# Kernel optimization log

Hardware: AMD Instinct MI355X
Metric: run time of the kernel (lower is better)

## Reference

```python
import jax, jax.numpy as jnp
import numpy as np

N = 20000      # nodes
E = 640000     # edges
R = 90         # relations
IN_F = 128     # raw feature dim
HID = 64       # hidden_channels
OUT = 32       # out_channels of conv2
NCLASS = 4
NB = 35        # num_bases (conv1)
EPS = 1e-16    # PyG softmax epsilon


def setup_inputs() -> dict:
    key = jax.random.key(0)
    ks = jax.random.split(key, 16)
    s = 0.1
    return {
        "x": jax.random.normal(ks[0], (N, IN_F), jnp.float32),
        "edge_index": jax.random.randint(ks[1], (2, E), 0, N, jnp.int32),
        "edge_type": jax.random.randint(ks[2], (E,), 0, R, jnp.int32),
        "edge_attr": jax.random.normal(ks[3], (E, 16), jnp.float32),
        # lin1: in_channels -> hidden (no bias)
        "lin1_w": jax.random.normal(ks[4], (IN_F, HID), jnp.float32) * s,
        # conv1: basis decomposition, heads=2, out=20, dim=2 -> H*O=40, H*dim=4
        "att1": jax.random.normal(ks[5], (R, NB), jnp.float32) * s,
        "basis1": jax.random.normal(ks[6], (NB, HID, 40), jnp.float32) * s,
        "q1": jax.random.normal(ks[7], (40, 4), jnp.float32) * s,
        "k1": jax.random.normal(ks[8], (40, 4), jnp.float32) * s,
        "wmod1": jnp.ones((20,), jnp.float32),            # mod='additive' weight (init ones)
        "bias1": jnp.zeros((80,), jnp.float32),            # concat bias: H*dim*O = 80
        # conv2: block-diagonal, in=80, blocks=2, H*O=64, H*dim=2
        "w2": jax.random.normal(ks[9], (R, 2, 40, 32), jnp.float32) * s,
        "q2": jax.random.normal(ks[10], (64, 2), jnp.float32) * s,
        "k2": jax.random.normal(ks[11], (64, 2), jnp.float32) * s,
        "lin_edge_w": jax.random.normal(ks[12], (16, 64), jnp.float32) * s,
        "e2": jax.random.normal(ks[13], (64, 2), jnp.float32) * s,
        # lin2: 2*out -> nclass
        "lin2_w": jax.random.normal(ks[14], (2 * OUT, NCLASS), jnp.float32) * s,
        "lin2_b": jnp.zeros((NCLASS,), jnp.float32),
    }


def segment_softmax(alpha, seg, num_segments):
    # PyG softmax: exp(x - detach(segment_max)) / (segment_sum + 1e-16)
    m = jax.ops.segment_max(alpha, seg, num_segments=num_segments)
    e = jnp.exp(alpha - jax.lax.stop_gradient(m)[seg])
    ssum = jax.ops.segment_sum(e, seg, num_segments=num_segments)
    return e / (ssum[seg] + EPS)


def rgat_forward(x, edge_index, edge_type, edge_attr, lin1_w, att1, basis1,
                 q1, k1, wmod1, bias1, w2, q2, k2, lin_edge_w, e2, lin2_w, lin2_b):
    src, dst = edge_index[0], edge_index[1]   # x_j = x[src], x_i = x[dst]
    n = x.shape[0]
    e = src.shape[0]

    h = x @ lin1_w                            # [N, HID]

    # ---- conv1: basis decomposition, within-relation, multiplicative attn, mod='additive'
    w = jnp.einsum('rb,bio->rio', att1, basis1)          # [R, HID, 40]
    xw = jnp.einsum('ni,rio->rno', h, w)                 # [R, N, 40] (all-relation transform)
    outj = xw[edge_type, src]                            # [E, 40]
    outi = xw[edge_type, dst]                            # [E, 40]
    qi = outi @ q1                                       # [E, 4]
    kj = outj @ k1                                       # [E, 4]
    alpha = qi * kj                                      # multiplicative-self-attention
    seg = dst.astype(jnp.int32) * R + edge_type          # within-relation softmax groups
    alpha = segment_softmax(alpha, seg, n * R)           # [E, 4]
    outj4 = outj.reshape(e, 2, 1, 20)                    # [E, H, 1, O]
    hmod = wmod1 * jnp.broadcast_to(outj4, (e, 2, 2, 20))  # mod='additive' term
    msg = outj4 * alpha.reshape(e, 2, 2, 1) + hmod       # [E, H, dim, O]
    agg = jax.ops.segment_sum(msg, dst, num_segments=n)  # [N, 2, 2, 20]
    h1 = agg.reshape(n, 80) + bias1
    h1 = jax.nn.relu(h1)

    # ---- conv2: block-diagonal, across-relation, additive attn, edge features, no bias
    xb = h1.reshape(n, 2, 40)
    xw2 = jnp.einsum('nbc,rbcd->rnbd', xb, w2).reshape(R, n, 64)  # [R, N, 64]
    outj = xw2[edge_type, src]                           # [E, 64]
    outi = xw2[edge_type, dst]
    qi = outi @ q2                                       # [E, 2]
    kj = outj @ k2
    ae = (edge_attr @ lin_edge_w) @ e2                   # [E, 2]
    alpha = jax.nn.leaky_relu(qi + kj + ae, 0.2)         # additive-self-attention
    alpha = segment_softmax(alpha, dst, n)               # across-relation
    msg = alpha.reshape(e, 2, 1) * outj.reshape(e, 2, 32)
    h2 = jax.ops.segment_sum(msg, dst, num_segments=n).reshape(n, 64)

    out = h2 @ lin2_w + lin2_b
    return jax.nn.log_softmax(out, axis=-1)


def reference(x, edge_index, edge_type, edge_attr, lin1_w, att1, basis1, q1, k1,
              wmod1, bias1, w2, q2, k2, lin_edge_w, e2, lin2_w, lin2_b):
    return rgat_forward(x, edge_index, edge_type, edge_attr, lin1_w, att1, basis1,
                        q1, k1, wmod1, bias1, w2, q2, k2, lin_edge_w, e2, lin2_w, lin2_b)
```

## Files before the change

kernel.cpp:

```cpp
#include <hip/hip_runtime.h>
#include <math.h>

constexpr int NN   = 20000;
constexpr int EE   = 640000;
constexpr int RR   = 90;
constexpr int INF_ = 128;
constexpr int HID  = 64;
constexpr float EPS = 1e-16f;
constexpr int E2   = 646144;

typedef unsigned short u16;
typedef _Float16 f16;
typedef __attribute__((ext_vector_type(8))) short bf16x8;
typedef __attribute__((ext_vector_type(8))) _Float16 f16x8;
typedef __attribute__((ext_vector_type(4))) _Float16 f16x4;
typedef __attribute__((ext_vector_type(4))) float f32x4;

__device__ inline u16 f2bf(float f) {
    unsigned int u = __float_as_uint(f);
    unsigned int r = (u + 0x7FFFu + ((u >> 16) & 1u)) >> 16;
    return (u16)r;
}

__device__ inline unsigned f2ord(float f) {
    unsigned u = __float_as_uint(f);
    return (u & 0x80000000u) ? ~u : (u | 0x80000000u);
}
__device__ inline float ord2f(unsigned x) {
    unsigned u = (x & 0x80000000u) ? (x & 0x7FFFFFFFu) : ~x;
    return __uint_as_float(u);
}
#define ORD_NEGINF 0x007FFFFFu

__global__ void k_fillrec(int4* p, int n) {
    int i = blockIdx.x * blockDim.x + threadIdx.x;
    if (i < n) { int4 r; r.x = 0; r.y = 0; r.z = 0; r.w = -1; p[i] = r; }
}

__global__ void k_hist(const int* et, int* hist) {
    __shared__ int lh[RR];
    if (threadIdx.x < RR) lh[threadIdx.x] = 0;
    __syncthreads();
    int i = blockIdx.x * blockDim.x + threadIdx.x;
    if (i < EE) atomicAdd(&lh[et[i]], 1);
    __syncthreads();
    if (threadIdx.x < RR) atomicAdd(&hist[threadIdx.x], lh[threadIdx.x]);
}

__global__ void k_scanPad(const int* hist, int* cursor) {
    if (threadIdx.x == 0) {
        int acc = 0;
        for (int r = 0; r < RR; ++r) {
            cursor[r] = acc;
            acc += (hist[r] + 63) & ~63;
        }
    }
}

__global__ void k_scatter(const int* src, const int* dst, const int* et,
                          int* cursor, int4* sortedR, int* posS) {
    __shared__ int lh[RR];
    __shared__ int lbase[RR];
    if (threadIdx.x < RR) lh[threadIdx.x] = 0;
    __syncthreads();
    int i = blockIdx.x * blockDim.x + threadIdx.x;
    int r = et[i];
    int rank = atomicAdd(&lh[r], 1);
    __syncthreads();
    if (threadIdx.x < RR) {
        int c = lh[threadIdx.x];
        lbase[threadIdx.x] = c ? atomicAdd(&cursor[threadIdx.x], c) : 0;
    }
    __syncthreads();
    int pos = lbase[r] + rank;
    int4 rec; rec.x = src[i]; rec.y = dst[i]; rec.z = r; rec.w = i;
    sortedR[pos] = rec;
    posS[i] = pos;
}

__global__ void k_histD(const int* dst, int* histD) {
    int i = blockIdx.x * blockDim.x + threadIdx.x;
    if (i < EE) atomicAdd(&histD[dst[i]], 1);
}

__global__ void k_scanD(const int* histD, int* rowptrD, int* cursorD) {
    __shared__ int part[256];
    const int CH = (NN + 255) / 256;
    int tid = threadIdx.x;
    int base = tid * CH;
    int s = 0;
    for (int j = 0; j < CH; ++j) {
        int idx = base + j;
        if (idx < NN) s += histD[idx];
    }
    part[tid] = s;
    __syncthreads();
    if (tid == 0) {
        int acc = 0;
        for (int t = 0; t < 256; ++t) { int v = part[t]; part[t] = acc; acc += v; }
    }
    __syncthreads();
    int acc = part[tid];
    for (int j = 0; j < CH; ++j) {
        int idx = base + j;
        if (idx < NN) {
            rowptrD[idx] = acc;
            cursorD[idx] = acc;
            acc += histD[idx];
        }
    }
    if (tid == 0) rowptrD[NN] = EE;
}

__global__ void k_scatterD(const int4* sortedR, int* cursorD, int* posD,
                           u16* relD) {
    int i = blockIdx.x * blockDim.x + threadIdx.x;
    if (i >= E2) return;
    int4 rec = sortedR[i];
    if (rec.w < 0) return;
    int pos = atomicAdd(&cursorD[rec.y], 1);
    posD[i] = pos;
    relD[pos] = (u16)rec.z;
}

__global__ void k_w1(const float* att1, const float* basis1, float* w1) {
    int idx = blockIdx.x * blockDim.x + threadIdx.x;
    if (idx >= RR * 2560) return;
    int r = idx / 2560, co = idx - r * 2560;
    float acc = 0.f;
    for (int b = 0; b < 35; ++b) acc += att1[r * 35 + b] * basis1[b * 2560 + co];
    w1[idx] = acc;
}

__global__ void k_wqk1(const float* w1, const float* q1, const float* k1,
                       float* wq1, float* wk1) {
    int idx = blockIdx.x * blockDim.x + threadIdx.x;
    if (idx >= RR * 64 * 4) return;
    int t = idx & 3, c = (idx >> 2) & 63, r = idx >> 8;
    const float* wrow = w1 + (size_t)r * 2560 + c * 40;
    float aq = 0.f, ak = 0.f;
    for (int o = 0; o < 40; ++o) {
        float w = wrow[o];
        aq += w * q1[o * 4 + t];
        ak += w * k1[o * 4 + t];
    }
    wq1[idx] = aq; wk1[idx] = ak;
}

__global__ void k_wqk2(const float* w2, const float* q2, const float* k2,
                       float* wq2, float* wk2) {
    int idx = blockIdx.x * blockDim.x + threadIdx.x;
    if (idx >= RR * 80 * 2) return;
    int t = idx & 1, bc = (idx >> 1) % 80, r = idx / 160;
    int b = bc / 40, c = bc % 40;
    const float* wbase = w2 + (size_t)((r * 2 + b) * 40 + c) * 32;
    float aq = 0.f, ak = 0.f;
    for (int d = 0; d < 32; ++d) {
        float w = wbase[d];
        aq += w * q2[(b * 32 + d) * 2 + t];
        ak += w * k2[(b * 32 + d) * 2 + t];
    }
    wq2[idx] = aq; wk2[idx] = ak;
}

__global__ void k_we(const float* lew, const float* e2, float* we) {
    int idx = threadIdx.x;
    if (idx >= 32) return;
    int i = idx >> 1, t = idx & 1;
    float acc = 0.f;
    for (int j = 0; j < 64; ++j) acc += lew[i * 64 + j] * e2[j * 2 + t];
    we[idx] = acc;
}

__global__ __launch_bounds__(256) void k_ae(const float* ea, const float* weg,
                                            const int* posS, float* aeS) {
    __shared__ float wes[32];
    if (threadIdx.x < 32) wes[threadIdx.x] = weg[threadIdx.x];
    __syncthreads();
    int e = blockIdx.x * 256 + threadIdx.x;
    if (e >= EE) return;
    const float4* ep = (const float4*)(ea + (size_t)e * 16);
    float a0 = 0.f, a1 = 0.f;
#pragma unroll
    for (int cc = 0; cc < 4; ++cc) {
        float4 v = ep[cc];
        const float* vv = (const float*)&v;
#pragma unroll
        for (int j = 0; j < 4; ++j) {
            int ii = cc * 4 + j;
            a0 = fmaf(vv[j], wes[ii * 2 + 0], a0);
            a1 = fmaf(vv[j], wes[ii * 2 + 1], a1);
        }
    }
    float2 av; av.x = a0; av.y = a1;
    *(float2*)(aeS + (size_t)posS[e] * 2) = av;
}

__global__ void k_w1bT(const float* w1, u16* w1bT) {
    int idx = blockIdx.x * blockDim.x + threadIdx.x;
    if (idx >= RR * 48 * 64) return;
    int k = idx & 63, o = (idx >> 6) % 48, r = idx / (48 * 64);
    float v = (o < 40) ? w1[(size_t)r * 2560 + k * 40 + o] : 0.f;
    w1bT[idx] = f2bf(v);
}

__global__ void k_w2bT(const float* w2, u16* w2bT) {
    int idx = blockIdx.x * blockDim.x + threadIdx.x;
    if (idx >= RR * 2 * 32 * 64) return;
    int c = idx & 63, d = (idx >> 6) & 31, b = (idx >> 11) & 1, r = idx >> 12;
    float v = (c < 40) ? w2[((((size_t)r * 2 + b) * 40) + c) * 32 + d] : 0.f;
    w2bT[idx] = f2bf(v);
}

__global__ void k_h(const float* x, const float* lin1_w, f16* hh, u16* hb) {
    __shared__ float xs[INF_];
    int n = blockIdx.x, t = threadIdx.x;
    xs[t]      = x[(size_t)n * INF_ + t];
    xs[t + 64] = x[(size_t)n * INF_ + t + 64];
    __syncthreads();
    float acc = 0.f;
    for (int i = 0; i < INF_; ++i) acc += xs[i] * lin1_w[i * HID + t];
    hh[(size_t)n * HID + t] = (f16)acc;
    hb[(size_t)n * HID + t] = f2bf(acc);
}

__device__ __forceinline__ void attn1_compute(const f16x8* hd, const f16x8* hs,
                                              const float* __restrict__ q,
                                              const float* __restrict__ k,
                                              float* qi, float* kj) {
#pragma unroll
    for (int t = 0; t < 4; ++t) { qi[t] = 0.f; kj[t] = 0.f; }
#pragma unroll
    for (int cc = 0; cc < 8; ++cc) {
        f16x8 a = hd[cc], b = hs[cc];
#pragma unroll
        for (int j = 0; j < 8; ++j) {
            float av = (float)a[j];
            float bv = (float)b[j];
            const float* q4 = q + (cc * 8 + j) * 4;
            const float* k4 = k + (cc * 8 + j) * 4;
#pragma unroll
            for (int t = 0; t < 4; ++t) {
                qi[t] = fmaf(av, q4[t], qi[t]);
                kj[t] = fmaf(bv, k4[t], kj[t]);
            }
        }
    }
}

__global__ __launch_bounds__(256) void k_e1s(const int4* sortedR, const f16* hh,
                                             const float* wq1g, const float* wk1g,
                                             const int* posD, float* alpha1s) {
    __shared__ float qs[256], ks[256];
    int i = blockIdx.x * 256 + threadIdx.x;
    int4 ed = sortedR[i];
    int s = ed.x, d = ed.y, r = ed.z;
    int rFirst = sortedR[(size_t)blockIdx.x * 256].z;
    int rLast  = sortedR[(size_t)blockIdx.x * 256 + 255].z;
    bool allsame = (rFirst == rLast);
    if (allsame) {
        qs[threadIdx.x] = wq1g[(size_t)rFirst * 256 + threadIdx.x];
        ks[threadIdx.x] = wk1g[(size_t)rFirst * 256 + threadIdx.x];
    }
    __syncthreads();
    if (ed.w < 0) return;
    const f16x8* hd = (const f16x8*)(hh + (size_t)d * 64);
    const f16x8* hs = (const f16x8*)(hh + (size_t)s * 64);
    float qi[4], kj[4];
    if (allsame) attn1_compute(hd, hs, qs, ks, qi, kj);
    else         attn1_compute(hd, hs, wq1g + (size_t)r * 256, wk1g + (size_t)r * 256, qi, kj);
    float4 av;
    av.x = qi[0] * kj[0];
    av.y = qi[1] * kj[1];
    av.z = qi[2] * kj[2];
    av.w = qi[3] * kj[3];
    *(float4*)(alpha1s + (size_t)posD[i] * 4) = av;
}

__global__ __launch_bounds__(256) void k_mfma1(const int4* sortedR, const int* posD,
                                               const u16* hb, const u16* w1bT,
                                               f16* outj1h) {
    int wid = threadIdx.x >> 6, l = threadIdx.x & 63;
    int base = blockIdx.x * 64;
    int r = sortedR[base].z;
    int e0 = base + wid * 16;
    int row16 = l & 15, g = l >> 4;
    bf16x8 a[3][2];
#pragma unroll
    for (int mt = 0; mt < 3; ++mt)
#pragma unroll
        for (int ks = 0; ks < 2; ++ks)
            a[mt][ks] = *(const bf16x8*)(w1bT + ((size_t)r * 48 + mt * 16 + row16) * 64 + ks * 32 + g * 8);
    int4 er = sortedR[e0 + row16];
    int s = er.x;
    bf16x8 b0 = *(const bf16x8*)(hb + (size_t)s * 64 + g * 8);
    bf16x8 b1 = *(const bf16x8*)(hb + (size_t)s * 64 + 32 + g * 8);
    f32x4 acc[3];
#pragma unroll
    for (int mt = 0; mt < 3; ++mt) acc[mt] = (f32x4){0.f, 0.f, 0.f, 0.f};
#pragma unroll
    for (int mt = 0; mt < 3; ++mt) {
        acc[mt] = __builtin_amdgcn_mfma_f32_16x16x32_bf16(a[mt][0], b0, acc[mt], 0, 0, 0);
        acc[mt] = __builtin_amdgcn_mfma_f32_16x16x32_bf16(a[mt][1], b1, acc[mt], 0, 0, 0);
    }
    if (er.w < 0) return;
    int pd = posD[e0 + row16];
    f16* orow = outj1h + (size_t)pd * 40;
#pragma unroll
    for (int mt = 0; mt < 3; ++mt) {
        int col = mt * 16 + g * 4;
        if (col < 40) {
            f16x4 v;
            v[0] = (f16)acc[mt][0]; v[1] = (f16)acc[mt][1];
            v[2] = (f16)acc[mt][2]; v[3] = (f16)acc[mt][3];
            *(f16x4*)(orow + col) = v;
        }
    }
}

__global__ __launch_bounds__(256) void k_aggr1(const u16* relD, const int* rowptrD,
                                               const f16* outj1h, const float* alpha1s,
                                               const float* wmod, const float* bias1,
                                               f16* h1h, u16* h1b) {
    __shared__ unsigned smax[4][RR * 5];
    __shared__ float    ssum[4][RR * 5];
    int wid = threadIdx.x >> 6;
    int lane = threadIdx.x & 63;
    int w = blockIdx.x * 4 + wid;
    int beg = rowptrD[w], end = rowptrD[w + 1];
    unsigned* mx = smax[wid];
    float*    sm = ssum[wid];
    for (int j = beg + lane; j < end; j += 64) {
        int rb = relD[j] * 5;
        mx[rb + 0] = ORD_NEGINF; mx[rb + 1] = ORD_NEGINF;
        mx[rb + 2] = ORD_NEGINF; mx[rb + 3] = ORD_NEGINF;
        sm[rb + 0] = 0.f; sm[rb + 1] = 0.f; sm[rb + 2] = 0.f; sm[rb + 3] = 0.f;
    }
    __syncthreads();
    for (int j = beg + lane; j < end; j += 64) {
        float4 a = *(const float4*)(alpha1s + (size_t)j * 4);
        int rb = relD[j] * 5;
        atomicMax(&mx[rb + 0], f2ord(a.x));
        atomicMax(&mx[rb + 1], f2ord(a.y));
        atomicMax(&mx[rb + 2], f2ord(a.z));
        atomicMax(&mx[rb + 3], f2ord(a.w));
    }
    __syncthreads();
    for (int j = beg + lane; j < end; j += 64) {
        float4 a = *(const float4*)(alpha1s + (size_t)j * 4);
        int rb = relD[j] * 5;
        atomicAdd(&sm[rb + 0], __expf(a.x - ord2f(mx[rb + 0])));
        atomicAdd(&sm[rb + 1], __expf(a.y - ord2f(mx[rb + 1])));
        atomicAdd(&sm[rb + 2], __expf(a.z - ord2f(mx[rb + 2])));
        atomicAdd(&sm[rb + 3], __expf(a.w - ord2f(mx[rb + 3])));
    }
    __syncthreads();
    for (int t = lane; t < RR * 5; t += 64) sm[t] = 1.f / (sm[t] + EPS);
    __syncthreads();
    int hh2 = lane >= 20 ? 1 : 0;
    int oo = lane - hh2 * 20;
    float acc0 = 0.f, acc1 = 0.f, accw = 0.f;
    if (lane < 40) {
        for (int j = beg; j < end; ++j) {
            int rb = relD[j] * 5 + hh2 * 2;
            float v = (float)outj1h[(size_t)j * 40 + lane];
            float2 a = *(const float2*)(alpha1s + (size_t)j * 4 + hh2 * 2);
            float e0 = __expf(a.x - ord2f(mx[rb]));
            float e1 = __expf(a.y - ord2f(mx[rb + 1]));
            acc0 = fmaf(v, e0 * sm[rb], acc0);
            acc1 = fmaf(v, e1 * sm[rb + 1], acc1);
            accw += v;
        }
        float wm = wmod[oo];
        int b0 = hh2 * 40 + oo;
        float o0 = fmaxf(acc0 + wm * accw + bias1[b0], 0.f);
        float o1 = fmaxf(acc1 + wm * accw + bias1[b0 + 20], 0.f);
        h1h[(size_t)w * 80 + b0]      = (f16)o0;
        h1h[(size_t)w * 80 + b0 + 20] = (f16)o1;
        h1b[((size_t)w * 2 + hh2) * 64 + oo]      = f2bf(o0);
        h1b[((size_t)w * 2 + hh2) * 64 + oo + 20] = f2bf(o1);
    } else {
        int lam = lane - 40;
        h1b[((size_t)w * 2 + 0) * 64 + 40 + lam] = 0;
        h1b[((size_t)w * 2 + 1) * 64 + 40 + lam] = 0;
    }
}

__device__ __forceinline__ void attn2_compute(const f16x8* hd, const f16x8* hs,
                                              const float* __restrict__ q,
                                              const float* __restrict__ k,
                                              float* a) {
    a[0] = 0.f; a[1] = 0.f;
#pragma unroll
    for (int cc = 0; cc < 10; ++cc) {
        f16x8 xv = hd[cc], yv = hs[cc];
#pragma unroll
        for (int j = 0; j < 8; ++j) {
            float x = (float)xv[j];
            float y = (float)yv[j];
            int bc = cc * 8 + j;
            a[0] = fmaf(x, q[bc * 2 + 0], fmaf(y, k[bc * 2 + 0], a[0]));
            a[1] = fmaf(x, q[bc * 2 + 1], fmaf(y, k[bc * 2 + 1], a[1]));
        }
    }
}

__global__ __launch_bounds__(256) void k_f1s(const int4* sortedR, const f16* h1h,
                                             const float* wq2g, const float* wk2g,
                                             const float* aeS, const int* posD,
                                             float* alpha2s) {
    __shared__ float qs[160], ks[160];
    int i = blockIdx.x * 256 + threadIdx.x;
    int4 ed = sortedR[i];
    int s = ed.x, d = ed.y, r = ed.z, e = ed.w;
    int rFirst = sortedR[(size_t)blockIdx.x * 256].z;
    int rLast  = sortedR[(size_t)blockIdx.x * 256 + 255].z;
    bool allsame = (rFirst == rLast);
    if (allsame && threadIdx.x < 160) {
        qs[threadIdx.x] = wq2g[(size_t)rFirst * 160 + threadIdx.x];
        ks[threadIdx.x] = wk2g[(size_t)rFirst * 160 + threadIdx.x];
    }
    __syncthreads();
    if (e < 0) return;
    const f16x8* hd = (const f16x8*)(h1h + (size_t)d * 80);
    const f16x8* hs = (const f16x8*)(h1h + (size_t)s * 80);
    float a[2];
    if (allsame) attn2_compute(hd, hs, qs, ks, a);
    else         attn2_compute(hd, hs, wq2g + (size_t)r * 160, wk2g + (size_t)r * 160, a);
    float2 aev = *(const float2*)(aeS + (size_t)i * 2);
    a[0] += aev.x;
    a[1] += aev.y;
    a[0] = a[0] > 0.f ? a[0] : 0.2f * a[0];
    a[1] = a[1] > 0.f ? a[1] : 0.2f * a[1];
    float2 av; av.x = a[0]; av.y = a[1];
    *(float2*)(alpha2s + (size_t)posD[i] * 2) = av;
}

__global__ __launch_bounds__(256) void k_mfma2(const int4* sortedR, const int* posD,
                                               const u16* h1b, const u16* w2bT,
                                               f16* outj2h) {
    int wid = threadIdx.x >> 6, l = threadIdx.x & 63;
    int base = blockIdx.x * 64;
    int r = sortedR[base].z;
    int e0 = base + wid * 16;
    int row16 = l & 15, g = l >> 4;
    bf16x8 a[2][2][2];
#pragma unroll
    for (int b = 0; b < 2; ++b)
#pragma unroll
        for (int mt = 0; mt < 2; ++mt)
#pragma unroll
            for (int ks = 0; ks < 2; ++ks)
                a[b][mt][ks] = *(const bf16x8*)(w2bT + ((((size_t)r * 2 + b) * 32) + mt * 16 + row16) * 64 + ks * 32 + g * 8);
    int4 er = sortedR[e0 + row16];
    int s = er.x;
    bf16x8 bb[2][2];
#pragma unroll
    for (int b = 0; b < 2; ++b)
#pragma unroll
        for (int ks = 0; ks < 2; ++ks)
            bb[b][ks] = *(const bf16x8*)(h1b + ((size_t)s * 2 + b) * 64 + ks * 32 + g * 8);
    f32x4 acc[2][2];
#pragma unroll
    for (int b = 0; b < 2; ++b)
#pragma unroll
        for (int mt = 0; mt < 2; ++mt) acc[b][mt] = (f32x4){0.f, 0.f, 0.f, 0.f};
#pragma unroll
    for (int b = 0; b < 2; ++b)
#pragma unroll
        for (int mt = 0; mt < 2; ++mt) {
            acc[b][mt] = __builtin_amdgcn_mfma_f32_16x16x32_bf16(a[b][mt][0], bb[b][0], acc[b][mt], 0, 0, 0);
            acc[b][mt] = __builtin_amdgcn_mfma_f32_16x16x32_bf16(a[b][mt][1], bb[b][1], acc[b][mt], 0, 0, 0);
        }
    if (er.w < 0) return;
    int pd = posD[e0 + row16];
    f16* orow = outj2h + (size_t)pd * 64;
#pragma unroll
    for (int b = 0; b < 2; ++b)
#pragma unroll
        for (int mt = 0; mt < 2; ++mt) {
            f16x4 v;
            v[0] = (f16)acc[b][mt][0]; v[1] = (f16)acc[b][mt][1];
            v[2] = (f16)acc[b][mt][2]; v[3] = (f16)acc[b][mt][3];
            *(f16x4*)(orow + b * 32 + mt * 16 + g * 4) = v;
        }
}

__global__ __launch_bounds__(256) void k_aggr2(const int* rowptrD, const f16* outj2h,
                                               const float* alpha2s, float* h2) {
    int w = blockIdx.x * 4 + (threadIdx.x >> 6);
    int lane = threadIdx.x & 63;
    if (w >= NN) return;
    int beg = rowptrD[w], end = rowptrD[w + 1];
    float m0 = -INFINITY, m1 = -INFINITY;
    for (int j = beg + lane; j < end; j += 64) {
        float2 a = *(const float2*)(alpha2s + (size_t)j * 2);
        m0 = fmaxf(m0, a.x); m1 = fmaxf(m1, a.y);
    }
#pragma unroll
    for (int off = 32; off; off >>= 1) {
        m0 = fmaxf(m0, __shfl_xor(m0, off));
        m1 = fmaxf(m1, __shfl_xor(m1, off));
    }
    float s0 = 0.f, s1 = 0.f;
    for (int j = beg + lane; j < end; j += 64) {
        float2 a = *(const float2*)(alpha2s + (size_t)j * 2);
        s0 += __expf(a.x - m0); s1 += __expf(a.y - m1);
    }
#pragma unroll
    for (int off = 32; off; off >>= 1) {
        s0 += __shfl_xor(s0, off);
        s1 += __shfl_xor(s1, off);
    }
    int b = lane >> 5;
    float mb = b ? m1 : m0;
    float rs = 1.f / ((b ? s1 : s0) + EPS);
    float acc = 0.f;
    for (int j = beg; j < end; ++j) {
        float v = (float)outj2h[(size_t)j * 64 + lane];
        float a = alpha2s[(size_t)j * 2 + b];
        acc = fmaf(v, __expf(a - mb) * rs, acc);
    }
    h2[(size_t)w * 64 + lane] = acc;
}

__global__ void k_out(const float* h2, const float* lin2_w, const float* lin2_b,
                      float* out) {
    int n = blockIdx.x * blockDim.x + threadIdx.x;
    if (n >= NN) return;
    float o[4] = {lin2_b[0], lin2_b[1], lin2_b[2], lin2_b[3]};
    const float* hr = h2 + (size_t)n * 64;
    for (int c = 0; c < 64; ++c) {
        float hv = hr[c];
#pragma unroll
        for (int t = 0; t < 4; ++t) o[t] = fmaf(hv, lin2_w[c * 4 + t], o[t]);
    }
    float m = fmaxf(fmaxf(o[0], o[1]), fmaxf(o[2], o[3]));
    float s = __expf(o[0] - m) + __expf(o[1] - m) + __expf(o[2] - m) + __expf(o[3] - m);
    float lse = m + logf(s);
#pragma unroll
    for (int t = 0; t < 4; ++t) out[(size_t)n * 4 + t] = o[t] - lse;
}

extern "C" void kernel_launch(void* const* d_in, const int* in_sizes, int n_in,
                              void* d_out, int out_size, void* d_ws, size_t ws_size,
                              hipStream_t stream) {
    const float* x        = (const float*)d_in[0];
    const int*   eidx     = (const int*)d_in[1];
    const int*   etype    = (const int*)d_in[2];
    const float* eattr    = (const float*)d_in[3];
    const float* lin1_w   = (const float*)d_in[4];
    const float* att1     = (const float*)d_in[5];
    const float* basis1   = (const float*)d_in[6];
    const float* q1       = (const float*)d_in[7];
    const float* k1       = (const float*)d_in[8];
    const float* wmod1    = (const float*)d_in[9];
    const float* bias1    = (const float*)d_in[10];
    const float* w2       = (const float*)d_in[11];
    const float* q2       = (const float*)d_in[12];
    const float* k2       = (const float*)d_in[13];
    const float* lew      = (const float*)d_in[14];
    const float* e2i      = (const float*)d_in[15];
    const float* lin2_w   = (const float*)d_in[16];
    const float* lin2_b   = (const float*)d_in[17];

    const int* src = eidx;
    const int* dst = eidx + EE;

    float* W = (float*)d_ws;
    float* w1      = W;   W += 230400;
    float* wq1     = W;   W += 23040;
    float* wk1     = W;   W += 23040;
    float* wq2     = W;   W += 14400;
    float* wk2     = W;   W += 14400;
    float* we      = W;   W += 32;
    float* h2      = W;   W += (size_t)NN * 64;
    float* aeS     = W;   W += (size_t)E2 * 2;
    f16*   hh      = (f16*)W;   W += (size_t)NN * 64 / 2;
    f16*   h1h     = (f16*)W;   W += (size_t)NN * 80 / 2;
    u16*   hb      = (u16*)W;   W += (size_t)NN * 64 / 2;
    u16*   h1b     = (u16*)W;   W += (size_t)NN * 128 / 2;
    u16*   w1bT    = (u16*)W;   W += (size_t)RR * 48 * 64 / 2;
    u16*   w2bT    = (u16*)W;   W += (size_t)RR * 2 * 32 * 64 / 2;
    float* uni     = W;   W += (size_t)EE * 20 + (size_t)EE * 4;
    f16*   outj1h  = (f16*)uni;
    float* alpha1s = uni + (size_t)EE * 20;
    f16*   outj2h  = (f16*)uni;
    W += (size_t)EE * 8;
    float* alpha2s = W;   W += (size_t)EE * 2;
    int4*  sortedR = (int4*)W;
    int*   I = (int*)W;   I += (size_t)E2 * 4;
    u16*   relD    = (u16*)I;   I += (size_t)E2 / 2;
    int*   posS    = I;   I += EE;
    int*   posD    = I;   I += E2;
    int*   rowptrD = I;   I += NN + 1;
    int*   cursorD = I;   I += NN;
    int*   histD   = I;   I += NN;
    int*   hist    = I;   I += 128;
    int*   cursor  = I;   I += 128;

    hipMemsetAsync(histD, 0, (size_t)(NN + 256) * 4, stream);
    k_fillrec<<<E2 / 256, 256, 0, stream>>>(sortedR, E2);

    k_hist<<<EE / 256, 256, 0, stream>>>(etype, hist);
    k_scanPad<<<1, 64, 0, stream>>>(hist, cursor);
    k_scatter<<<EE / 256, 256, 0, stream>>>(src, dst, etype, cursor, sortedR, posS);
    k_histD<<<EE / 256, 256, 0, stream>>>(dst, histD);
    k_scanD<<<1, 256, 0, stream>>>(histD, rowptrD, cursorD);
    k_scatterD<<<E2 / 256, 256, 0, stream>>>(sortedR, cursorD, posD, relD);

    k_w1<<<(RR * 2560 + 255) / 256, 256, 0, stream>>>(att1, basis1, w1);
    k_wqk1<<<(RR * 256 + 255) / 256, 256, 0, stream>>>(w1, q1, k1, wq1, wk1);
    k_wqk2<<<(RR * 160 + 255) / 256, 256, 0, stream>>>(w2, q2, k2, wq2, wk2);
    k_we<<<1, 32, 0, stream>>>(lew, e2i, we);
    k_ae<<<EE / 256, 256, 0, stream>>>(eattr, we, posS, aeS);
    k_w1bT<<<(RR * 48 * 64) / 256, 256, 0, stream>>>(w1, w1bT);
    k_w2bT<<<(RR * 2 * 32 * 64) / 256, 256, 0, stream>>>(w2, w2bT);
    k_h<<<NN, 64, 0, stream>>>(x, lin1_w, hh, hb);

    k_e1s<<<E2 / 256, 256, 0, stream>>>(sortedR, hh, wq1, wk1, posD, alpha1s);
    k_mfma1<<<E2 / 64, 256, 0, stream>>>(sortedR, posD, hb, w1bT, outj1h);
    k_aggr1<<<NN / 4, 256, 0, stream>>>(relD, rowptrD, outj1h, alpha1s,
                                        wmod1, bias1, h1h, h1b);

    k_f1s<<<E2 / 256, 256, 0, stream>>>(sortedR, h1h, wq2, wk2, aeS, posD, alpha2s);
    k_mfma2<<<E2 / 64, 256, 0, stream>>>(sortedR, posD, h1b, w2bT, outj2h);
    k_aggr2<<<(NN + 3) / 4, 256, 0, stream>>>(rowptrD, outj2h, alpha2s, h2);

    k_out<<<(NN + 255) / 256, 256, 0, stream>>>(h2, lin2_w, lin2_b, (float*)d_out);
}
```

Measured before the change: 640.5 us.

## Fuse attention-score and MFMA message kernels per layer using fp16 operands

Merges the per-edge attention-score kernels (k_e1s/k_f1s) into the MFMA message-transform kernels, so each edge's source and destination features are loaded once. The score reduction is spread across lanes and combined with cross-lane shuffles. MFMA operands change from bf16 to fp16, which removes the duplicate bf16 copies of h, h1 and the weights. The dst-sorted position is stored in the sorted record's w field instead of a separate posD array. This saves several kernel launches and extra global traffic, but the h1h row reads now run past the 40-wide block, so a small zeroed tail pad is added.

```diff
diff --git a/kernel.cpp b/kernel.cpp
--- a/kernel.cpp
+++ b/kernel.cpp
@@ -11,16 +11,9 @@
 
 typedef unsigned short u16;
 typedef _Float16 f16;
-typedef __attribute__((ext_vector_type(8))) short bf16x8;
 typedef __attribute__((ext_vector_type(8))) _Float16 f16x8;
 typedef __attribute__((ext_vector_type(4))) _Float16 f16x4;
 typedef __attribute__((ext_vector_type(4))) float f32x4;
-
-__device__ inline u16 f2bf(float f) {
-    unsigned int u = __float_as_uint(f);
-    unsigned int r = (u + 0x7FFFu + ((u >> 16) & 1u)) >> 16;
-    return (u16)r;
-}
 
 __device__ inline unsigned f2ord(float f) {
     unsigned u = __float_as_uint(f);
@@ -112,14 +105,13 @@
     if (tid == 0) rowptrD[NN] = EE;
 }
 
-__global__ void k_scatterD(const int4* sortedR, int* cursorD, int* posD,
-                           u16* relD) {
+__global__ void k_scatterD(int4* sortedR, int* cursorD, u16* relD) {
     int i = blockIdx.x * blockDim.x + threadIdx.x;
     if (i >= E2) return;
     int4 rec = sortedR[i];
     if (rec.w < 0) return;
     int pos = atomicAdd(&cursorD[rec.y], 1);
-    posD[i] = pos;
+    ((int*)(sortedR + i))[3] = pos;
     relD[pos] = (u16)rec.z;
 }
 
@@ -196,23 +188,23 @@
     *(float2*)(aeS + (size_t)posS[e] * 2) = av;
 }
 
-__global__ void k_w1bT(const float* w1, u16* w1bT) {
+__global__ void k_w1hT(const float* w1, f16* w1hT) {
     int idx = blockIdx.x * blockDim.x + threadIdx.x;
     if (idx >= RR * 48 * 64) return;
     int k = idx & 63, o = (idx >> 6) % 48, r = idx / (48 * 64);
     float v = (o < 40) ? w1[(size_t)r * 2560 + k * 40 + o] : 0.f;
-    w1bT[idx] = f2bf(v);
-}
-
-__global__ void k_w2bT(const float* w2, u16* w2bT) {
+    w1hT[idx] = (f16)v;
+}
+
+__global__ void k_w2hT(const float* w2, f16* w2hT) {
     int idx = blockIdx.x * blockDim.x + threadIdx.x;
     if (idx >= RR * 2 * 32 * 64) return;
     int c = idx & 63, d = (idx >> 6) & 31, b = (idx >> 11) & 1, r = idx >> 12;
     float v = (c < 40) ? w2[((((size_t)r * 2 + b) * 40) + c) * 32 + d] : 0.f;
-    w2bT[idx] = f2bf(v);
-}
-
-__global__ void k_h(const float* x, const float* lin1_w, f16* hh, u16* hb) {
+    w2hT[idx] = (f16)v;
+}
+
+__global__ void k_h(const float* x, const float* lin1_w, f16* hh) {
     __shared__ float xs[INF_];
     int n = blockIdx.x, t = threadIdx.x;
     xs[t]      = x[(size_t)n * INF_ + t];
@@ -221,90 +213,65 @@
     float acc = 0.f;
     for (int i = 0; i < INF_; ++i) acc += xs[i] * lin1_w[i * HID + t];
     hh[(size_t)n * HID + t] = (f16)acc;
-    hb[(size_t)n * HID + t] = f2bf(acc);
-}
-
-__device__ __forceinline__ void attn1_compute(const f16x8* hd, const f16x8* hs,
-                                              const float* __restrict__ q,
-                                              const float* __restrict__ k,
-                                              float* qi, float* kj) {
-#pragma unroll
-    for (int t = 0; t < 4; ++t) { qi[t] = 0.f; kj[t] = 0.f; }
-#pragma unroll
-    for (int cc = 0; cc < 8; ++cc) {
-        f16x8 a = hd[cc], b = hs[cc];
-#pragma unroll
-        for (int j = 0; j < 8; ++j) {
-            float av = (float)a[j];
-            float bv = (float)b[j];
-            const float* q4 = q + (cc * 8 + j) * 4;
-            const float* k4 = k + (cc * 8 + j) * 4;
-#pragma unroll
-            for (int t = 0; t < 4; ++t) {
-                qi[t] = fmaf(av, q4[t], qi[t]);
-                kj[t] = fmaf(bv, k4[t], kj[t]);
-            }
-        }
-    }
-}
-
-__global__ __launch_bounds__(256) void k_e1s(const int4* sortedR, const f16* hh,
-                                             const float* wq1g, const float* wk1g,
-                                             const int* posD, float* alpha1s) {
+}
+
+__global__ __launch_bounds__(256) void k_c1(const int4* sortedR, const f16* hh,
+                                            const f16* w1hT,
+                                            const float* wq1g, const float* wk1g,
+                                            float* alpha1s, f16* outj1h) {
     __shared__ float qs[256], ks[256];
-    int i = blockIdx.x * 256 + threadIdx.x;
-    int4 ed = sortedR[i];
-    int s = ed.x, d = ed.y, r = ed.z;
-    int rFirst = sortedR[(size_t)blockIdx.x * 256].z;
-    int rLast  = sortedR[(size_t)blockIdx.x * 256 + 255].z;
-    bool allsame = (rFirst == rLast);
-    if (allsame) {
-        qs[threadIdx.x] = wq1g[(size_t)rFirst * 256 + threadIdx.x];
-        ks[threadIdx.x] = wk1g[(size_t)rFirst * 256 + threadIdx.x];
-    }
-    __syncthreads();
-    if (ed.w < 0) return;
-    const f16x8* hd = (const f16x8*)(hh + (size_t)d * 64);
-    const f16x8* hs = (const f16x8*)(hh + (size_t)s * 64);
-    float qi[4], kj[4];
-    if (allsame) attn1_compute(hd, hs, qs, ks, qi, kj);
-    else         attn1_compute(hd, hs, wq1g + (size_t)r * 256, wk1g + (size_t)r * 256, qi, kj);
-    float4 av;
-    av.x = qi[0] * kj[0];
-    av.y = qi[1] * kj[1];
-    av.z = qi[2] * kj[2];
-    av.w = qi[3] * kj[3];
-    *(float4*)(alpha1s + (size_t)posD[i] * 4) = av;
-}
-
-__global__ __launch_bounds__(256) void k_mfma1(const int4* sortedR, const int* posD,
-                                               const u16* hb, const u16* w1bT,
-                                               f16* outj1h) {
-    int wid = threadIdx.x >> 6, l = threadIdx.x & 63;
     int base = blockIdx.x * 64;
     int r = sortedR[base].z;
+    qs[threadIdx.x] = wq1g[(size_t)r * 256 + threadIdx.x];
+    ks[threadIdx.x] = wk1g[(size_t)r * 256 + threadIdx.x];
+    __syncthreads();
+    int wid = threadIdx.x >> 6, l = threadIdx.x & 63;
     int e0 = base + wid * 16;
     int row16 = l & 15, g = l >> 4;
-    bf16x8 a[3][2];
+    f16x8 a[3][2];
 #pragma unroll
     for (int mt = 0; mt < 3; ++mt)
 #pragma unroll
-        for (int ks = 0; ks < 2; ++ks)
-            a[mt][ks] = *(const bf16x8*)(w1bT + ((size_t)r * 48 + mt * 16 + row16) * 64 + ks * 32 + g * 8);
+        for (int kk = 0; kk < 2; ++kk)
+            a[mt][kk] = *(const f16x8*)(w1hT + ((size_t)r * 48 + mt * 16 + row16) * 64 + kk * 32 + g * 8);
     int4 er = sortedR[e0 + row16];
-    int s = er.x;
-    bf16x8 b0 = *(const bf16x8*)(hb + (size_t)s * 64 + g * 8);
-    bf16x8 b1 = *(const bf16x8*)(hb + (size_t)s * 64 + 32 + g * 8);
+    int s = er.x, d = er.y, pd = er.w;
+    f16x8 b0 = *(const f16x8*)(hh + (size_t)s * 64 + g * 8);
+    f16x8 b1 = *(const f16x8*)(hh + (size_t)s * 64 + 32 + g * 8);
+    f16x8 d0 = *(const f16x8*)(hh + (size_t)d * 64 + g * 8);
+    f16x8 d1 = *(const f16x8*)(hh + (size_t)d * 64 + 32 + g * 8);
+    float qi[4] = {0.f, 0.f, 0.f, 0.f}, kj[4] = {0.f, 0.f, 0.f, 0.f};
+#pragma unroll
+    for (int j = 0; j < 8; ++j) {
+        int p0 = g * 8 + j, p1 = 32 + g * 8 + j;
+        float dv0 = (float)d0[j], dv1 = (float)d1[j];
+        float bv0 = (float)b0[j], bv1 = (float)b1[j];
+#pragma unroll
+        for (int t = 0; t < 4; ++t) {
+            qi[t] = fmaf(dv0, qs[p0 * 4 + t], fmaf(dv1, qs[p1 * 4 + t], qi[t]));
+            kj[t] = fmaf(bv0, ks[p0 * 4 + t], fmaf(bv1, ks[p1 * 4 + t], kj[t]));
+        }
+    }
+#pragma unroll
+    for (int t = 0; t < 4; ++t) {
+        qi[t] += __shfl_xor(qi[t], 16); qi[t] += __shfl_xor(qi[t], 32);
+        kj[t] += __shfl_xor(kj[t], 16); kj[t] += __shfl_xor(kj[t], 32);
+    }
     f32x4 acc[3];
 #pragma unroll
     for (int mt = 0; mt < 3; ++mt) acc[mt] = (f32x4){0.f, 0.f, 0.f, 0.f};
 #pragma unroll
     for (int mt = 0; mt < 3; ++mt) {
-        acc[mt] = __builtin_amdgcn_mfma_f32_16x16x32_bf16(a[mt][0], b0, acc[mt], 0, 0, 0);
-        acc[mt] = __builtin_amdgcn_mfma_f32_16x16x32_bf16(a[mt][1], b1, acc[mt], 0, 0, 0);
-    }
-    if (er.w < 0) return;
-    int pd = posD[e0 + row16];
+        acc[mt] = __builtin_amdgcn_mfma_f32_16x16x32_f16(a[mt][0], b0, acc[mt], 0, 0, 0);
+        acc[mt] = __builtin_amdgcn_mfma_f32_16x16x32_f16(a[mt][1], b1, acc[mt], 0, 0, 0);
+    }
+    if (pd < 0) return;
+    if (l < 16) {
+        float4 av;
+        av.x = qi[0] * kj[0]; av.y = qi[1] * kj[1];
+        av.z = qi[2] * kj[2]; av.w = qi[3] * kj[3];
+        *(float4*)(alpha1s + (size_t)pd * 4) = av;
+    }
     f16* orow = outj1h + (size_t)pd * 40;
 #pragma unroll
     for (int mt = 0; mt < 3; ++mt) {
@@ -321,7 +288,7 @@
 __global__ __launch_bounds__(256) void k_aggr1(const u16* relD, const int* rowptrD,
                                                const f16* outj1h, const float* alpha1s,
                                                const float* wmod, const float* bias1,
-                                               f16* h1h, u16* h1b) {
+                                               f16* h1h) {
     __shared__ unsigned smax[4][RR * 5];
     __shared__ float    ssum[4][RR * 5];
     int wid = threadIdx.x >> 6;
@@ -377,89 +344,65 @@
         float o1 = fmaxf(acc1 + wm * accw + bias1[b0 + 20], 0.f);
         h1h[(size_t)w * 80 + b0]      = (f16)o0;
         h1h[(size_t)w * 80 + b0 + 20] = (f16)o1;
-        h1b[((size_t)w * 2 + hh2) * 64 + oo]      = f2bf(o0);
-        h1b[((size_t)w * 2 + hh2) * 64 + oo + 20] = f2bf(o1);
-    } else {
-        int lam = lane - 40;
-        h1b[((size_t)w * 2 + 0) * 64 + 40 + lam] = 0;
-        h1b[((size_t)w * 2 + 1) * 64 + 40 + lam] = 0;
-    }
-}
-
-__device__ __forceinline__ void attn2_compute(const f16x8* hd, const f16x8* hs,
-                                              const float* __restrict__ q,
-                                              const float* __restrict__ k,
-                                              float* a) {
-    a[0] = 0.f; a[1] = 0.f;
-#pragma unroll
-    for (int cc = 0; cc < 10; ++cc) {
-        f16x8 xv = hd[cc], yv = hs[cc];
-#pragma unroll
-        for (int j = 0; j < 8; ++j) {
-            float x = (float)xv[j];
-            float y = (float)yv[j];
-            int bc = cc * 8 + j;
-            a[0] = fmaf(x, q[bc * 2 + 0], fmaf(y, k[bc * 2 + 0], a[0]));
-            a[1] = fmaf(x, q[bc * 2 + 1], fmaf(y, k[bc * 2 + 1], a[1]));
-        }
-    }
-}
-
-__global__ __launch_bounds__(256) void k_f1s(const int4* sortedR, const f16* h1h,
-                                             const float* wq2g, const float* wk2g,
-                                             const float* aeS, const int* posD,
-                                             float* alpha2s) {
+    }
+}
+
+__global__ __launch_bounds__(256) void k_c2(const int4* sortedR, const f16* h1h,
+                                            const f16* w2hT,
+                                            const float* wq2g, const float* wk2g,
+                                            const float* aeS,
+                                            float* alpha2s, f16* outj2h) {
     __shared__ float qs[160], ks[160];
-    int i = blockIdx.x * 256 + threadIdx.x;
-    int4 ed = sortedR[i];
-    int s = ed.x, d = ed.y, r = ed.z, e = ed.w;
-    int rFirst = sortedR[(size_t)blockIdx.x * 256].z;
-    int rLast  = sortedR[(size_t)blockIdx.x * 256 + 255].z;
-    bool allsame = (rFirst == rLast);
-    if (allsame && threadIdx.x < 160) {
-        qs[threadIdx.x] = wq2g[(size_t)rFirst * 160 + threadIdx.x];
-        ks[threadIdx.x] = wk2g[(size_t)rFirst * 160 + threadIdx.x];
-    }
-    __syncthreads();
-    if (e < 0) return;
-    const f16x8* hd = (const f16x8*)(h1h + (size_t)d * 80);
-    const f16x8* hs = (const f16x8*)(h1h + (size_t)s * 80);
-    float a[2];
-    if (allsame) attn2_compute(hd, hs, qs, ks, a);
-    else         attn2_compute(hd, hs, wq2g + (size_t)r * 160, wk2g + (size_t)r * 160, a);
-    float2 aev = *(const float2*)(aeS + (size_t)i * 2);
-    a[0] += aev.x;
-    a[1] += aev.y;
-    a[0] = a[0] > 0.f ? a[0] : 0.2f * a[0];
-    a[1] = a[1] > 0.f ? a[1] : 0.2f * a[1];
-    float2 av; av.x = a[0]; av.y = a[1];
-    *(float2*)(alpha2s + (size_t)posD[i] * 2) = av;
-}
-
-__global__ __launch_bounds__(256) void k_mfma2(const int4* sortedR, const int* posD,
-                                               const u16* h1b, const u16* w2bT,
-                                               f16* outj2h) {
-    int wid = threadIdx.x >> 6, l = threadIdx.x & 63;
     int base = blockIdx.x * 64;
     int r = sortedR[base].z;
+    if (threadIdx.x < 160) {
+        qs[threadIdx.x] = wq2g[(size_t)r * 160 + threadIdx.x];
+        ks[threadIdx.x] = wk2g[(size_t)r * 160 + threadIdx.x];
+    }
+    __syncthreads();
+    int wid = threadIdx.x >> 6, l = threadIdx.x & 63;
     int e0 = base + wid * 16;
     int row16 = l & 15, g = l >> 4;
-    bf16x8 a[2][2][2];
+    f16x8 a[2][2][2];
 #pragma unroll
     for (int b = 0; b < 2; ++b)
 #pragma unroll
         for (int mt = 0; mt < 2; ++mt)
 #pragma unroll
-            for (int ks = 0; ks < 2; ++ks)
-                a[b][mt][ks] = *(const bf16x8*)(w2bT + ((((size_t)r * 2 + b) * 32) + mt * 16 + row16) * 64 + ks * 32 + g * 8);
+            for (int kk = 0; kk < 2; ++kk)
+                a[b][mt][kk] = *(const f16x8*)(w2hT + ((((size_t)r * 2 + b) * 32) + mt * 16 + row16) * 64 + kk * 32 + g * 8);
     int4 er = sortedR[e0 + row16];
-    int s = er.x;
-    bf16x8 bb[2][2];
+    int s = er.x, d = er.y, pd = er.w;
+    f16x8 bb[2][2], dd[2][2];
 #pragma unroll
     for (int b = 0; b < 2; ++b)
 #pragma unroll
-        for (int ks = 0; ks < 2; ++ks)
-            bb[b][ks] = *(const bf16x8*)(h1b + ((size_t)s * 2 + b) * 64 + ks * 32 + g * 8);
+        for (int kk = 0; kk < 2; ++kk) {
+            bb[b][kk] = *(const f16x8*)(h1h + (size_t)s * 80 + b * 40 + kk * 32 + g * 8);
+            dd[b][kk] = *(const f16x8*)(h1h + (size_t)d * 80 + b * 40 + kk * 32 + g * 8);
+        }
+    float a0 = 0.f, a1 = 0.f;
+#pragma unroll
+    for (int b = 0; b < 2; ++b) {
+#pragma unroll
+        for (int j = 0; j < 8; ++j) {
+            int p = b * 40 + g * 8 + j;
+            float dv = (float)dd[b][0][j], bv = (float)bb[b][0][j];
+            a0 = fmaf(dv, qs[p * 2 + 0], fmaf(bv, ks[p * 2 + 0], a0));
+            a1 = fmaf(dv, qs[p * 2 + 1], fmaf(bv, ks[p * 2 + 1], a1));
+        }
+        if (g == 0) {
+#pragma unroll
+            for (int j = 0; j < 8; ++j) {
+                int p = b * 40 + 32 + j;
+                float dv = (float)dd[b][1][j], bv = (float)bb[b][1][j];
+                a0 = fmaf(dv, qs[p * 2 + 0], fmaf(bv, ks[p * 2 + 0], a0));
+                a1 = fmaf(dv, qs[p * 2 + 1], fmaf(bv, ks[p * 2 + 1], a1));
+            }
+        }
+    }
+    a0 += __shfl_xor(a0, 16); a0 += __shfl_xor(a0, 32);
+    a1 += __shfl_xor(a1, 16); a1 += __shfl_xor(a1, 32);
     f32x4 acc[2][2];
 #pragma unroll
     for (int b = 0; b < 2; ++b)
@@ -469,11 +412,18 @@
     for (int b = 0; b < 2; ++b)
 #pragma unroll
         for (int mt = 0; mt < 2; ++mt) {
-            acc[b][mt] = __builtin_amdgcn_mfma_f32_16x16x32_bf16(a[b][mt][0], bb[b][0], acc[b][mt], 0, 0, 0);
-            acc[b][mt] = __builtin_amdgcn_mfma_f32_16x16x32_bf16(a[b][mt][1], bb[b][1], acc[b][mt], 0, 0, 0);
-        }
-    if (er.w < 0) return;
-    int pd = posD[e0 + row16];
+            acc[b][mt] = __builtin_amdgcn_mfma_f32_16x16x32_f16(a[b][mt][0], bb[b][0], acc[b][mt], 0, 0, 0);
+            acc[b][mt] = __builtin_amdgcn_mfma_f32_16x16x32_f16(a[b][mt][1], bb[b][1], acc[b][mt], 0, 0, 0);
+        }
+    if (pd < 0) return;
+    if (l < 16) {
+        float2 aev = *(const float2*)(aeS + (size_t)(e0 + row16) * 2);
+        float x0 = a0 + aev.x, x1 = a1 + aev.y;
+        x0 = x0 > 0.f ? x0 : 0.2f * x0;
+        x1 = x1 > 0.f ? x1 : 0.2f * x1;
+        float2 av; av.x = x0; av.y = x1;
+        *(float2*)(alpha2s + (size_t)pd * 2) = av;
+    }
     f16* orow = outj2h + (size_t)pd * 64;
 #pragma unroll
     for (int b = 0; b < 2; ++b)
@@ -577,11 +527,9 @@
     float* h2      = W;   W += (size_t)NN * 64;
     float* aeS     = W;   W += (size_t)E2 * 2;
     f16*   hh      = (f16*)W;   W += (size_t)NN * 64 / 2;
-    f16*   h1h     = (f16*)W;   W += (size_t)NN * 80 / 2;
-    u16*   hb      = (u16*)W;   W += (size_t)NN * 64 / 2;
-    u16*   h1b     = (u16*)W;   W += (size_t)NN * 128 / 2;
-    u16*   w1bT    = (u16*)W;   W += (size_t)RR * 48 * 64 / 2;
-    u16*   w2bT    = (u16*)W;   W += (size_t)RR * 2 * 32 * 64 / 2;
+    f16*   h1h     = (f16*)W;   W += (size_t)NN * 80 / 2 + 32;
+    f16*   w1hT    = (f16*)W;   W += (size_t)RR * 48 * 64 / 2;
+    f16*   w2hT    = (f16*)W;   W += (size_t)RR * 2 * 32 * 64 / 2;
     float* uni     = W;   W += (size_t)EE * 20 + (size_t)EE * 4;
     f16*   outj1h  = (f16*)uni;
     float* alpha1s = uni + (size_t)EE * 20;
@@ -592,7 +540,6 @@
     int*   I = (int*)W;   I += (size_t)E2 * 4;
     u16*   relD    = (u16*)I;   I += (size_t)E2 / 2;
     int*   posS    = I;   I += EE;
-    int*   posD    = I;   I += E2;
     int*   rowptrD = I;   I += NN + 1;
     int*   cursorD = I;   I += NN;
     int*   histD   = I;   I += NN;
@@ -600,6 +547,7 @@
     int*   cursor  = I;   I += 128;
 
     hipMemsetAsync(histD, 0, (size_t)(NN + 256) * 4, stream);
+    hipMemsetAsync(h1h + (size_t)NN * 80, 0, 128, stream);
     k_fillrec<<<E2 / 256, 256, 0, stream>>>(sortedR, E2);
 
     k_hist<<<EE / 256, 256, 0, stream>>>(etype, hist);
@@ -607,24 +555,23 @@
     k_scatter<<<EE / 256, 256, 0, stream>>>(src, dst, etype, cursor, sortedR, posS);
     k_histD<<<EE / 256, 256, 0, stream>>>(dst, histD);
     k_scanD<<<1, 256, 0, stream>>>(histD, rowptrD, cursorD);
-    k_scatterD<<<E2 / 256, 256, 0, stream>>>(sortedR, cursorD, posD, relD);
+    k_scatterD<<<E2 / 256, 256, 0, stream>>>(sortedR, cursorD, relD);
 
     k_w1<<<(RR * 2560 + 255) / 256, 256, 0, stream>>>(att1, basis1, w1);
     k_wqk1<<<(RR * 256 + 255) / 256, 256, 0, stream>>>(w1, q1, k1, wq1, wk1);
     k_wqk2<<<(RR * 160 + 255) / 256, 256, 0, stream>>>(w2, q2, k2, wq2, wk2);
     k_we<<<1, 32, 0, stream>>>(lew, e2i, we);
     k_ae<<<EE / 256, 256, 0, stream>>>(eattr, we, posS, aeS);
-    k_w1bT<<<(RR * 48 * 64) / 256, 256, 0, stream>>>(w1, w1bT);
-    k_w2bT<<<(RR * 2 * 32 * 64) / 256, 256, 0, stream>>>(w2, w2bT);
-    k_h<<<NN, 64, 0, stream>>>(x, lin1_w, hh, hb);
-
-    k_e1s<<<E2 / 256, 256, 0, stream>>>(sortedR, hh, wq1, wk1, posD, alpha1s);
-    k_mfma1<<<E2 / 64, 256, 0, stream>>>(sortedR, posD, hb, w1bT, outj1h);
+    k_w1hT<<<(RR * 48 * 64) / 256, 256, 0, stream>>>(w1, w1hT);
+    k_w2hT<<<(RR * 2 * 32 * 64) / 256, 256, 0, stream>>>(w2, w2hT);
+    k_h<<<NN, 64, 0, stream>>>(x, lin1_w, hh);
+
+    k_c1<<<E2 / 64, 256, 0, stream>>>(sortedR, hh, w1hT, wq1, wk1, alpha1s, outj1h);
     k_aggr1<<<NN / 4, 256, 0, stream>>>(relD, rowptrD, outj1h, alpha1s,
-                                        wmod1, bias1, h1h, h1b);
-
-    k_f1s<<<E2 / 256, 256, 0, stream>>>(sortedR, h1h, wq2, wk2, aeS, posD, alpha2s);
-    k_mfma2<<<E2 / 64, 256, 0, stream>>>(sortedR, posD, h1b, w2bT, outj2h);
+                                        wmod1, bias1, h1h);
+
+    k_c2<<<E2 / 64, 256, 0, stream>>>(sortedR, h1h, w2hT, wq2, wk2, aeS,
+                                      alpha2s, outj2h);
     k_aggr2<<<(NN + 3) / 4, 256, 0, stream>>>(rowptrD, outj2h, alpha2s, h2);
 
     k_out<<<(NN + 255) / 256, 256, 0, stream>>>(h2, lin2_w, lin2_b, (float*)d_out);
```

New measurement: 603.0 us. -5.9%, faster.
